# Performance work log

Hardware: AMD Instinct MI355X
Metric: run time of the kernel (lower is better)

Reference implementation:

```python
import jax, jax.numpy as jnp
import numpy as np

N_HEAD = 16

def setup_inputs() -> dict:
    key = jax.random.key(0)
    k0, k1, k2, k3, k4 = jax.random.split(key, 5)
    B, T, C = 4, 2048, 1024
    x = jax.random.normal(k0, (B, T, C), dtype=jnp.float32)
    # torch nn.Linear weights are (out_features, in_features); scale like kaiming-uniform-ish
    s = 1.0 / np.sqrt(C)
    Wk = jax.random.uniform(k1, (C, C), jnp.float32, -s, s)
    Wq = jax.random.uniform(k2, (C, C), jnp.float32, -s, s)
    Wv = jax.random.uniform(k3, (C, C), jnp.float32, -s, s)
    Wo = jax.random.uniform(k4, (C, C), jnp.float32, -s, s)
    return {"x": x, "Wk": Wk, "Wq": Wq, "Wv": Wv, "Wo": Wo}

def reference(x, Wk, Wq, Wv, Wo):
    B, T, C = x.shape
    hs = C // N_HEAD
    # projections (torch Linear: y = x @ W.T), split heads -> (B, nh, T, hs)
    def proj(W):
        return (x @ W.T).reshape(B, T, N_HEAD, hs).transpose(0, 2, 1, 3)
    k = proj(Wk)
    q = proj(Wq)
    v = proj(Wv)
    # dot attention: scale by sqrt(head_dim) (k.shape[2] after transpose in source)
    score = jnp.einsum('bhqd,bhkd->bhqk', q, k) / jnp.sqrt(jnp.asarray(hs, x.dtype))
    # NOTE: source calls score.masked_fill(mask, -inf) without assignment -> mask has no effect.
    e = jax.nn.softmax(score, axis=-1)
    o = jnp.einsum('bhqk,bhkd->bhqd', e, v)          # (B, nh, T, hs)
    o = o.transpose(0, 2, 1, 3).reshape(B, T, C)     # merge heads
    o = o @ Wo.T                                      # final projection
    # dropout is identity in eval mode
    return o
```

## Files before the change

kernel.cpp:

```cpp
#include <hip/hip_runtime.h>
#include <hip/hip_bf16.h>
#include <cstddef>
#include <cstdint>

#define B_DIM 4
#define T_DIM 2048
#define C_DIM 1024
#define NHEAD 16
#define HS    64
#define QKV_LD 3072

#define QSCALE 0.18033688011112042f

typedef __attribute__((ext_vector_type(8))) short short8;
typedef __attribute__((ext_vector_type(4))) float f32x4;

__device__ __forceinline__ short f2bf(float x) {
    __hip_bfloat16 b = __float2bfloat16(x);
    return *reinterpret_cast<short*>(&b);
}

__device__ __forceinline__ void load_lds16(const void* g, void* l) {
    __builtin_amdgcn_global_load_lds(
        (const __attribute__((address_space(1))) void*)(g),
        (__attribute__((address_space(3))) void*)(l),
        16, 0, 0);
}

__global__ __launch_bounds__(256) void cast_bf16(
    const float* __restrict__ in, short* __restrict__ out, int n8, float scale)
{
    int i = blockIdx.x * 256 + threadIdx.x;
    if (i >= n8) return;
    const float4* p = (const float4*)in + (size_t)i * 2;
    float4 a = p[0], b = p[1];
    short8 o;
    o[0]=f2bf(a.x*scale); o[1]=f2bf(a.y*scale); o[2]=f2bf(a.z*scale); o[3]=f2bf(a.w*scale);
    o[4]=f2bf(b.x*scale); o[5]=f2bf(b.y*scale); o[6]=f2bf(b.z*scale); o[7]=f2bf(b.w*scale);
    *((short8*)out + i) = o;
}

#define BM 128
#define BN 128
#define BK 32

template<bool OUT_BF16>
__global__ __launch_bounds__(256) void gemm_bt_mfma(
    const short* __restrict__ A,
    const short* __restrict__ Bm,
    void* __restrict__ Cm,
    int M, int N, int K, float scale)
{
    __shared__ __align__(16) short smem[8192];
    short* As = smem;
    short* Bs = smem + 4096;

    const int m0 = blockIdx.y * BM;
    const int n0 = blockIdx.x * BN;
    const int t    = threadIdx.x;
    const int w    = t >> 6;
    const int lane = t & 63;
    const int l16  = lane & 15;
    const int quad = lane >> 4;
    const int wm   = w >> 1;
    const int wn   = w & 1;

    const int mS0 = t >> 2;
    const int qS  = (t & 3) ^ ((t >> 3) & 3);
    const short* aG0 = A  + (size_t)(m0 + mS0)      * K + qS * 8;
    const short* aG1 = A  + (size_t)(m0 + mS0 + 64) * K + qS * 8;
    const short* bG0 = Bm + (size_t)(n0 + mS0)      * K + qS * 8;
    const short* bG1 = Bm + (size_t)(n0 + mS0 + 64) * K + qS * 8;
    short* aL0 = As + (size_t)(w * 64) * 8;
    short* aL1 = As + (size_t)(256 + w * 64) * 8;
    short* bL0 = Bs + (size_t)(w * 64) * 8;
    short* bL1 = Bs + (size_t)(256 + w * 64) * 8;

    int a_off[4], b_off[4];
    #pragma unroll
    for (int i = 0; i < 4; ++i) {
        int am = wm * 64 + i * 16 + l16;
        a_off[i] = (am * 4 + (quad ^ ((am >> 1) & 3))) * 8;
        int bn = wn * 64 + i * 16 + l16;
        b_off[i] = (bn * 4 + (quad ^ ((bn >> 1) & 3))) * 8;
    }

    f32x4 acc[4][4];
    const f32x4 zero4 = {0.f, 0.f, 0.f, 0.f};
    #pragma unroll
    for (int i = 0; i < 4; ++i)
        #pragma unroll
        for (int j = 0; j < 4; ++j) acc[i][j] = zero4;

    for (int k0 = 0; k0 < K; k0 += BK) {
        __syncthreads();
        load_lds16(aG0 + k0, aL0);
        load_lds16(aG1 + k0, aL1);
        load_lds16(bG0 + k0, bL0);
        load_lds16(bG1 + k0, bL1);
        __syncthreads();

        short8 af[4], bf[4];
        #pragma unroll
        for (int i = 0; i < 4; ++i) {
            af[i] = *(const short8*)(As + a_off[i]);
            bf[i] = *(const short8*)(Bs + b_off[i]);
        }
        #pragma unroll
        for (int i = 0; i < 4; ++i)
            #pragma unroll
            for (int j = 0; j < 4; ++j)
                acc[i][j] = __builtin_amdgcn_mfma_f32_16x16x32_bf16(
                    af[i], bf[j], acc[i][j], 0, 0, 0);
    }

    #pragma unroll
    for (int i = 0; i < 4; ++i) {
        const int row_base = m0 + wm * 64 + i * 16 + quad * 4;
        #pragma unroll
        for (int j = 0; j < 4; ++j) {
            const int col = n0 + wn * 64 + j * 16 + l16;
            #pragma unroll
            for (int r = 0; r < 4; ++r) {
                const size_t idx = (size_t)(row_base + r) * N + col;
                if (OUT_BF16) ((short*)Cm)[idx] = f2bf(acc[i][j][r] * scale);
                else          ((float*)Cm)[idx] = acc[i][j][r] * scale;
            }
        }
    }
}

__global__ __launch_bounds__(256) void transpose_v(
    const short* __restrict__ Vb,
    short* __restrict__ Vt, int srcLD)
{
    const int t0 = blockIdx.x * 64;
    const int head = blockIdx.y;
    const int b = head >> 4, h = head & 15;

    __shared__ short Ls[64][72];

    const int t = threadIdx.x;
    const int r = t >> 2;
    const int c = (t & 3) * 16;

    const short* src = Vb + ((size_t)(b * T_DIM) + t0 + r) * srcLD + h * HS + c;
    *(short8*)&Ls[r][c]     = *(const short8*)src;
    *(short8*)&Ls[r][c + 8] = *(const short8*)(src + 8);
    __syncthreads();

    short tmp[16];
    #pragma unroll
    for (int i = 0; i < 16; ++i) tmp[i] = Ls[c + i][r];
    short* dst = Vt + ((size_t)head * HS + r) * T_DIM + t0 + c;
    *(short8*)dst       = *(short8*)&tmp[0];
    *(short8*)(dst + 8) = *(short8*)&tmp[8];
}

#define QSUB 4

__global__ __launch_bounds__(256, 2) void attn_mfma3(
    const short* __restrict__ Qb,
    const short* __restrict__ Kb,
    const short* __restrict__ Vt,
    short* __restrict__ O)
{
    const int i0   = blockIdx.x * (64 * QSUB);
    const int head = blockIdx.y;
    const int b = head >> 4, h = head & 15;

    const int t    = threadIdx.x;
    const int w    = t >> 6;
    const int lane = t & 63;
    const int l16  = lane & 15;
    const int quad = lane >> 4;

    __shared__ short Ks[64][72];
    __shared__ short Vts[64][72];

    short8 qf[QSUB][2];
    #pragma unroll
    for (int sub = 0; sub < QSUB; ++sub) {
        const short* qrow = Qb
            + ((size_t)(b * T_DIM) + i0 + sub * 64 + w * 16 + l16) * QKV_LD + h * HS;
        qf[sub][0] = *(const short8*)(qrow + quad * 8);
        qf[sub][1] = *(const short8*)(qrow + 32 + quad * 8);
    }

    short8 onesv;
    #pragma unroll
    for (int j = 0; j < 8; ++j) onesv[j] = (short)0x3F80;

    const f32x4 zero4 = {0.f, 0.f, 0.f, 0.f};
    f32x4 oacc[QSUB][4];
    f32x4 lacc[QSUB];
    #pragma unroll
    for (int sub = 0; sub < QSUB; ++sub) {
        #pragma unroll
        for (int dg = 0; dg < 4; ++dg) oacc[sub][dg] = zero4;
        lacc[sub] = zero4;
    }

    const int sr = t >> 2;
    const int sc = (t & 3) * 16;
    const int krow = (sr & 32) | ((sr & 4) << 2) | ((sr & 24) >> 1) | (sr & 3);
    const short* kgbase = Kb + (size_t)(b * T_DIM) * QKV_LD + h * HS;
    const short* vgbase = Vt + ((size_t)head * HS + sr) * T_DIM;

    for (int j0 = 0; j0 < T_DIM; j0 += 64) {
        __syncthreads();
        {
            const short* kp = kgbase + (size_t)(j0 + sr) * QKV_LD + sc;
            *(short8*)&Ks[krow][sc]     = *(const short8*)kp;
            *(short8*)&Ks[krow][sc + 8] = *(const short8*)(kp + 8);
            const short* vp = vgbase + j0 + sc;
            *(short8*)&Vts[sr][sc]      = *(const short8*)vp;
            *(short8*)&Vts[sr][sc + 8]  = *(const short8*)(vp + 8);
        }
        __syncthreads();

        short8 ka[4][2], va[4][2];
        #pragma unroll
        for (int kt = 0; kt < 4; ++kt) {
            ka[kt][0] = *(const short8*)&Ks[kt * 16 + l16][quad * 8];
            ka[kt][1] = *(const short8*)&Ks[kt * 16 + l16][32 + quad * 8];
            va[kt][0] = *(const short8*)&Vts[kt * 16 + l16][quad * 8];
            va[kt][1] = *(const short8*)&Vts[kt * 16 + l16][32 + quad * 8];
        }

        #pragma unroll
        for (int sub = 0; sub < QSUB; ++sub) {
            f32x4 s[4];
            #pragma unroll
            for (int kt = 0; kt < 4; ++kt) {
                f32x4 acc = zero4;
                acc = __builtin_amdgcn_mfma_f32_16x16x32_bf16(ka[kt][0], qf[sub][0], acc, 0, 0, 0);
                acc = __builtin_amdgcn_mfma_f32_16x16x32_bf16(ka[kt][1], qf[sub][1], acc, 0, 0, 0);
                s[kt] = acc;
            }

            short8 pa[2];
            #pragma unroll
            for (int hh = 0; hh < 2; ++hh) {
                #pragma unroll
                for (int c = 0; c < 2; ++c) {
                    f32x4 sv = s[2 * hh + c];
                    #pragma unroll
                    for (int r = 0; r < 4; ++r) {
                        float p = __builtin_amdgcn_exp2f(sv[r]);
                        pa[hh][c * 4 + r] = f2bf(p);
                    }
                }
            }

            lacc[sub] = __builtin_amdgcn_mfma_f32_16x16x32_bf16(pa[0], onesv, lacc[sub], 0, 0, 0);
            lacc[sub] = __builtin_amdgcn_mfma_f32_16x16x32_bf16(pa[1], onesv, lacc[sub], 0, 0, 0);

            #pragma unroll
            for (int dg = 0; dg < 4; ++dg) {
                oacc[sub][dg] = __builtin_amdgcn_mfma_f32_16x16x32_bf16(pa[0], va[dg][0], oacc[sub][dg], 0, 0, 0);
                oacc[sub][dg] = __builtin_amdgcn_mfma_f32_16x16x32_bf16(pa[1], va[dg][1], oacc[sub][dg], 0, 0, 0);
            }
        }
    }

    #pragma unroll
    for (int sub = 0; sub < QSUB; ++sub) {
        float linv[4];
        #pragma unroll
        for (int r = 0; r < 4; ++r) linv[r] = 1.0f / lacc[sub][r];

        #pragma unroll
        for (int r = 0; r < 4; ++r) {
            short* orow = O + ((size_t)(b * T_DIM) + i0 + sub * 64 + w * 16 + quad * 4 + r) * C_DIM + h * HS;
            #pragma unroll
            for (int dg = 0; dg < 4; ++dg)
                orow[dg * 16 + l16] = f2bf(oacc[sub][dg][r] * linv[r]);
        }
    }
}

extern "C" void kernel_launch(void* const* d_in, const int* in_sizes, int n_in,
                              void* d_out, int out_size, void* d_ws, size_t ws_size,
                              hipStream_t stream) {
    const float* x  = (const float*)d_in[0];
    const float* Wk = (const float*)d_in[1];
    const float* Wq = (const float*)d_in[2];
    const float* Wv = (const float*)d_in[3];
    const float* Wo = (const float*)d_in[4];
    float* out = (float*)d_out;

    const int M = B_DIM * T_DIM;
    const size_t NE = (size_t)M * C_DIM;
    const size_t NB = 2 * NE;
    const size_t WB = (size_t)2 * C_DIM * C_DIM;
    const size_t WE = (size_t)C_DIM * C_DIM;

    char* ws = (char*)d_ws;
    short* xb   = (short*)(ws);
    short* Ob   = xb;
    short* QKVb = (short*)(ws + NB);
    short* Vtb  = (short*)(ws + 4 * NB);
    short* W3b  = (short*)(ws + 5 * NB);
    short* Wob  = (short*)(ws + 5 * NB + 3 * WB);

    cast_bf16<<<(int)(NE / 8 / 256), 256, 0, stream>>>(x, xb, (int)(NE / 8), 1.0f);
    const int wn8 = (int)(WE / 8);
    cast_bf16<<<wn8 / 256, 256, 0, stream>>>(Wq, W3b,          wn8, QSCALE);
    cast_bf16<<<wn8 / 256, 256, 0, stream>>>(Wk, W3b + WE,     wn8, 1.0f);
    cast_bf16<<<wn8 / 256, 256, 0, stream>>>(Wv, W3b + 2 * WE, wn8, 1.0f);
    cast_bf16<<<wn8 / 256, 256, 0, stream>>>(Wo, Wob,          wn8, 1.0f);

    gemm_bt_mfma<true><<<dim3(QKV_LD / BN, M / BM), 256, 0, stream>>>(
        xb, W3b, QKVb, M, QKV_LD, C_DIM, 1.0f);

    transpose_v<<<dim3(T_DIM / 64, B_DIM * NHEAD), 256, 0, stream>>>(
        QKVb + 2 * C_DIM, Vtb, QKV_LD);

    attn_mfma3<<<dim3(T_DIM / (64 * QSUB), B_DIM * NHEAD), 256, 0, stream>>>(
        QKVb, QKVb + C_DIM, Vtb, Ob);

    gemm_bt_mfma<false><<<dim3(C_DIM / BN, M / BM), 256, 0, stream>>>(
        Ob, Wob, out, M, C_DIM, C_DIM, 1.0f);
}
```

Baseline: 278.0 us.

## Replace QKV projection GEMM with 256x256-tile, 8-wave, phased-prefetch MFMA kernel

Adds a new bf16 GEMM kernel for the fused QKV projection. It uses 256x256 output tiles, 512 threads, a 64-wide K step, an XOR-swizzled LDS layout, and double-buffered direct global-to-LDS loads spread across four compute phases. A block-index remap groups workgroups for better L2 locality, and s_setprio is raised around the MFMA bursts. The aim is more operand reuse and better overlap of loads with matrix math than the old 128x128 kernel. The cost is much higher LDS use (128KB per block) and register pressure, plus extra barriers.

```diff
diff --git a/kernel.cpp b/kernel.cpp
--- a/kernel.cpp
+++ b/kernel.cpp
@@ -40,6 +40,137 @@
     *((short8*)out + i) = o;
 }
 
+__global__ __launch_bounds__(512, 2) void gemm_bt_8ph(
+    const short* __restrict__ A,
+    const short* __restrict__ Bm,
+    short* __restrict__ Cm,
+    int M, int N, int K)
+{
+    __shared__ __align__(16) short lds[65536];
+
+    const int nbx = N >> 8;
+    int wg = blockIdx.x;
+    const int cpx = gridDim.x >> 3;
+    wg = (wg & 7) * cpx + (wg >> 3);
+    const int bx = wg % nbx, by = wg / nbx;
+    const int m0 = by << 8, n0 = bx << 8;
+
+    const int t = threadIdx.x;
+    const int w = t >> 6, lane = t & 63;
+    const int l16 = lane & 15, quad = lane >> 4;
+    const int wm = w >> 2, wn = w & 3;
+
+    const int rcall  = t >> 3;
+    const int chunk  = t & 7;
+    const int schunk = chunk ^ (rcall & 7);
+    const int dstrow = w * 8;
+
+    const short* AgT = A  + (size_t)(m0 + rcall) * K + schunk * 8;
+    const short* AgB = AgT + (size_t)128 * K;
+    const short* BgT = Bm + (size_t)(n0 + rcall) * K + schunk * 8;
+    const short* BgB = BgT + (size_t)128 * K;
+
+    int aoff[8][2], boff[4][2];
+    #pragma unroll
+    for (int mf = 0; mf < 8; ++mf) {
+        const int ar = wm * 128 + mf * 16 + l16;
+        #pragma unroll
+        for (int ks = 0; ks < 2; ++ks)
+            aoff[mf][ks] = ar * 64 + (((ks * 4 + quad) ^ (ar & 7)) * 8);
+    }
+    #pragma unroll
+    for (int nf = 0; nf < 4; ++nf) {
+        const int br = wn * 64 + nf * 16 + l16;
+        #pragma unroll
+        for (int ks = 0; ks < 2; ++ks)
+            boff[nf][ks] = br * 64 + (((ks * 4 + quad) ^ (br & 7)) * 8);
+    }
+
+    f32x4 acc[8][4];
+    const f32x4 zero4 = {0.f, 0.f, 0.f, 0.f};
+    #pragma unroll
+    for (int mf = 0; mf < 8; ++mf)
+        #pragma unroll
+        for (int nf = 0; nf < 4; ++nf) acc[mf][nf] = zero4;
+
+    const int NT = K >> 6;
+
+    #define STAGE_HALF(gbase, kt, lhalf)                                        \
+        {                                                                        \
+            load_lds16((gbase) + (size_t)(kt) * 64,                              \
+                       (lhalf) + dstrow * 64);                                   \
+            load_lds16((gbase) + (size_t)64 * K + (size_t)(kt) * 64,             \
+                       (lhalf) + (64 + dstrow) * 64);                            \
+        }
+
+    STAGE_HALF(AgT, 0, lds);
+    STAGE_HALF(AgB, 0, lds + 128 * 64);
+    STAGE_HALF(BgT, 0, lds + 32768);
+    STAGE_HALF(BgB, 0, lds + 32768 + 128 * 64);
+    STAGE_HALF(AgT, 1, lds + 16384);
+
+    for (int kt = 0; kt < NT; ++kt) {
+        const int b0 = kt & 1;
+        const short* Acur = lds + b0 * 16384;
+        const short* Bcur = lds + 32768 + b0 * 16384;
+        short* Anx = lds + (b0 ^ 1) * 16384;
+        short* Bnx = lds + 32768 + (b0 ^ 1) * 16384;
+
+        if (kt == NT - 1) asm volatile("s_waitcnt vmcnt(0)" ::: "memory");
+        else              asm volatile("s_waitcnt vmcnt(2)" ::: "memory");
+        __builtin_amdgcn_s_barrier();
+
+        short8 bfr[4][2];
+        #pragma unroll
+        for (int nf = 0; nf < 4; ++nf)
+            #pragma unroll
+            for (int ks = 0; ks < 2; ++ks)
+                bfr[nf][ks] = *(const short8*)(Bcur + boff[nf][ks]);
+
+        #pragma unroll
+        for (int ph = 0; ph < 4; ++ph) {
+            short8 af[2][2];
+            #pragma unroll
+            for (int r = 0; r < 2; ++r)
+                #pragma unroll
+                for (int ks = 0; ks < 2; ++ks)
+                    af[r][ks] = *(const short8*)(Acur + aoff[ph * 2 + r][ks]);
+
+            if (ph == 0)      { if (kt + 1 < NT) STAGE_HALF(AgB, kt + 1, Anx + 128 * 64); }
+            else if (ph == 1) { if (kt + 1 < NT) STAGE_HALF(BgT, kt + 1, Bnx); }
+            else if (ph == 2) { if (kt + 1 < NT) STAGE_HALF(BgB, kt + 1, Bnx + 128 * 64); }
+
+            __builtin_amdgcn_s_barrier();
+            __builtin_amdgcn_s_setprio(1);
+            #pragma unroll
+            for (int r = 0; r < 2; ++r)
+                #pragma unroll
+                for (int nf = 0; nf < 4; ++nf)
+                    #pragma unroll
+                    for (int ks = 0; ks < 2; ++ks)
+                        acc[ph * 2 + r][nf] = __builtin_amdgcn_mfma_f32_16x16x32_bf16(
+                            af[r][ks], bfr[nf][ks], acc[ph * 2 + r][nf], 0, 0, 0);
+            __builtin_amdgcn_s_setprio(0);
+            __builtin_amdgcn_s_barrier();
+        }
+
+        if (kt + 2 < NT) { short* Aw = lds + b0 * 16384; STAGE_HALF(AgT, kt + 2, Aw); }
+    }
+    #undef STAGE_HALF
+
+    #pragma unroll
+    for (int mf = 0; mf < 8; ++mf) {
+        const int row_base = m0 + wm * 128 + mf * 16 + quad * 4;
+        #pragma unroll
+        for (int nf = 0; nf < 4; ++nf) {
+            const int col = n0 + wn * 64 + nf * 16 + l16;
+            #pragma unroll
+            for (int r = 0; r < 4; ++r)
+                Cm[(size_t)(row_base + r) * N + col] = f2bf(acc[mf][nf][r]);
+        }
+    }
+}
+
 #define BM 128
 #define BN 128
 #define BK 32
@@ -311,8 +442,8 @@
     cast_bf16<<<wn8 / 256, 256, 0, stream>>>(Wv, W3b + 2 * WE, wn8, 1.0f);
     cast_bf16<<<wn8 / 256, 256, 0, stream>>>(Wo, Wob,          wn8, 1.0f);
 
-    gemm_bt_mfma<true><<<dim3(QKV_LD / BN, M / BM), 256, 0, stream>>>(
-        xb, W3b, QKVb, M, QKV_LD, C_DIM, 1.0f);
+    gemm_bt_8ph<<<dim3((QKV_LD / 256) * (M / 256)), 512, 0, stream>>>(
+        xb, W3b, QKVb, M, QKV_LD, C_DIM);
 
     transpose_v<<<dim3(T_DIM / 64, B_DIM * NHEAD), 256, 0, stream>>>(
         QKVb + 2 * C_DIM, Vtb, QKV_LD);
```

Measured after the change: 269.3 us. 3.1% less time.
